# Performance work log

Hardware: AMD Instinct MI355X
Metric: run time of the kernel (lower is better)

Reference implementation:

```python
import jax, jax.numpy as jnp
import numpy as np

B, L = 1, 2048
D_MODEL, D_STATE, D_CONV, EXPAND = 512, 16, 4, 2
D_INNER = D_MODEL * EXPAND
EPS = 1e-10  # clamp used by the torch reference


def setup_inputs() -> dict:
    key = jax.random.key(0)
    ks = jax.random.split(key, 8)
    s = lambda fan: 1.0 / np.sqrt(fan)
    x = jax.random.normal(ks[0], (B, L, D_MODEL), jnp.float32)
    # Weights stored in (in, out) layout: y = x @ W  (equivalent to torch Linear with W.T)
    W_in = jax.random.normal(ks[1], (D_MODEL, 2 * D_INNER), jnp.float32) * s(D_MODEL)
    conv_w = jax.random.normal(ks[2], (D_INNER, 1, D_CONV), jnp.float32) * s(D_CONV)  # depthwise (O, I/groups, K)
    conv_b = jax.random.normal(ks[3], (D_INNER,), jnp.float32) * 0.01
    W_xproj = jax.random.normal(ks[4], (D_INNER, 2 * D_STATE + 1), jnp.float32) * s(D_INNER)
    dt_w = jax.random.normal(ks[5], (D_INNER,), jnp.float32) * 0.1  # Linear(1, d_inner) weight, squeezed
    dt_b = jax.random.normal(ks[6], (D_INNER,), jnp.float32) * 0.1 - 2.0  # keep delta smallish
    A_log = jnp.log(jnp.arange(1, D_STATE + 1, dtype=jnp.float32))
    D = jnp.ones((D_INNER,), jnp.float32)
    W_out = jax.random.normal(ks[7], (D_INNER, D_MODEL), jnp.float32) * s(D_INNER)
    return {"x": x, "W_in": W_in, "conv_w": conv_w, "conv_b": conv_b,
            "W_xproj": W_xproj, "dt_w": dt_w, "dt_b": dt_b,
            "A_log": A_log, "D": D, "W_out": W_out}


def reference(x, W_in, conv_w, conv_b, W_xproj, dt_w, dt_b, A_log, D, W_out):
    d_inner, _, d_conv = conv_w.shape
    d_state = A_log.shape[0]

    xz = x @ W_in                                    # (B, L, 2*d_inner)
    xs, z = jnp.split(xz, 2, axis=-1)

    # Depthwise causal conv1d: left-pad d_conv-1 == torch pad-both + truncate to L
    xc = jnp.transpose(xs, (0, 2, 1))                # (B, d_inner, L)
    xc = jax.lax.conv_general_dilated(
        xc, conv_w, window_strides=(1,), padding=[(d_conv - 1, 0)],
        feature_group_count=d_inner,
        dimension_numbers=("NCH", "OIH", "NCH")) + conv_b[None, :, None]
    xs = jax.nn.silu(jnp.transpose(xc, (0, 2, 1)))   # (B, L, d_inner)

    xp = xs @ W_xproj                                # (B, L, 2*d_state+1)
    delta = jax.nn.softplus(xp[..., 0:1] * dt_w + dt_b)  # (B, L, d_inner)
    Bp = xp[..., 1:1 + d_state]                      # (B, L, d_state)
    Cp = xp[..., 1 + d_state:]                       # (B, L, d_state)
    A = -jnp.exp(A_log)                              # (d_state,)

    # --- parallel selective scan via cumulative log-sum (faithful to source) ---
    A_bar = jnp.exp(delta[..., None] * A)                            # (B,L,Di,S)
    BX = delta[..., None] * Bp[:, :, None, :] * xs[..., None]        # (B,L,Di,S)
    log_A_bar = jnp.log(jnp.maximum(A_bar, EPS))
    A_cumsum = jnp.exp(jnp.cumsum(log_A_bar, axis=1))
    A_shift = jnp.concatenate([jnp.ones_like(A_cumsum[:, :1]), A_cumsum[:, :-1]], axis=1)
    weighted_BX = BX / jnp.maximum(A_shift, EPS)
    h = A_cumsum * jnp.cumsum(weighted_BX, axis=1) / jnp.maximum(A_bar, EPS)
    y = jnp.einsum("bls,blds->bld", Cp, h) + D * xs                  # (B,L,Di)

    y = y * jax.nn.silu(z)
    return y @ W_out                                                  # (B,L,D)
```

## Files before the change

kernel.cpp:

```cpp
#include <hip/hip_runtime.h>
#include <hip/hip_bf16.h>


#define L_SEQ 2048
#define DM 512
#define DI 1024
#define DS 16
#define NXP 33
#define EPS 1e-10f
#define RCPEPS 1e10f
#define LOG2E 1.44269504088896340736f
#define LN2 0.69314718055994530942f
#define LOG2EPS -33.219280948873623478f

typedef __hip_bfloat16 bf16;
typedef __attribute__((ext_vector_type(8))) short bf16x8v;
typedef __attribute__((ext_vector_type(4))) float f32x4v;
typedef __attribute__((ext_vector_type(4))) unsigned int u32x4v;

__device__ __forceinline__ float ldf(const float* p) { return *p; }
__device__ __forceinline__ float ldf(const bf16* p) { return __bfloat162float(*p); }

__device__ __forceinline__ void st1(float* p, float v) { *p = v; }
__device__ __forceinline__ void st1(bf16* p, float v) { *p = __float2bfloat16(v); }

__device__ __forceinline__ float fexp2(float x) { return __builtin_amdgcn_exp2f(x); }
__device__ __forceinline__ float frcp(float x) { return __builtin_amdgcn_rcpf(x); }

__device__ __forceinline__ void load8(const float* p, float* v) {
  float4 a = *(const float4*)p;
  float4 b = *(const float4*)(p + 4);
  v[0] = a.x; v[1] = a.y; v[2] = a.z; v[3] = a.w;
  v[4] = b.x; v[5] = b.y; v[6] = b.z; v[7] = b.w;
}
__device__ __forceinline__ void load8(const bf16* p, float* v) {
  bf16 t[8];
  *(uint4*)t = *(const uint4*)p;
#pragma unroll
  for (int j = 0; j < 8; ++j) v[j] = __bfloat162float(t[j]);
}

__global__ __launch_bounds__(256)
void transpose_cast_kernel(const float* __restrict__ W, bf16* __restrict__ WT,
                           int R, int C) {
  __shared__ float tile[32][33];
  int c0 = blockIdx.x * 32, r0 = blockIdx.y * 32;
  int tx = threadIdx.x & 31, ty = threadIdx.x >> 5;
#pragma unroll
  for (int i = 0; i < 4; ++i) {
    int rr = ty + i * 8;
    tile[rr][tx] = W[(size_t)(r0 + rr) * C + c0 + tx];
  }
  __syncthreads();
#pragma unroll
  for (int i = 0; i < 4; ++i) {
    int cc = ty + i * 8;
    WT[(size_t)(c0 + cc) * R + r0 + tx] = __float2bfloat16(tile[tx][cc]);
  }
}

__global__ __launch_bounds__(256)
void cast_f32_bf16_kernel(const float* __restrict__ src, bf16* __restrict__ dst,
                          int n8) {
  int i = blockIdx.x * 256 + threadIdx.x;
  if (i < n8) {
    float v[8];
    load8(src + (size_t)i * 8, v);
    bf16 o[8];
#pragma unroll
    for (int j = 0; j < 8; ++j) o[j] = __float2bfloat16(v[j]);
    *(uint4*)(dst + (size_t)i * 8) = *(uint4*)o;
  }
}

template <typename TA, typename TC>
__global__ __launch_bounds__(256)
void gemm_bt64(const TA* __restrict__ A, const bf16* __restrict__ BT,
               TC* __restrict__ C, int M, int N, int K, int lda, int ldc) {
  __shared__ __align__(16) bf16 As[64 * 40];
  __shared__ __align__(16) bf16 Bs[64 * 40];
  const int tid = threadIdx.x;
  const int wave = tid >> 6, lane = tid & 63;
  const int q = lane >> 4, r = lane & 15;
  const int row0 = blockIdx.y * 64, col0 = blockIdx.x * 64;
  const int srow = tid >> 2, sseg = tid & 3;
  f32x4v acc[4] = {};
  for (int k0 = 0; k0 < K; k0 += 32) {
    if constexpr (sizeof(TA) == 2) {
      *(uint4*)&As[srow * 40 + sseg * 8] =
          *(const uint4*)(A + (size_t)(row0 + srow) * lda + k0 + sseg * 8);
    } else {
      float v[8];
      load8(A + (size_t)(row0 + srow) * lda + k0 + sseg * 8, v);
      bf16* dst = &As[srow * 40 + sseg * 8];
#pragma unroll
      for (int j = 0; j < 8; ++j) dst[j] = __float2bfloat16(v[j]);
    }
    *(uint4*)&Bs[srow * 40 + sseg * 8] =
        *(const uint4*)(BT + (size_t)(col0 + srow) * K + k0 + sseg * 8);
    __syncthreads();
    bf16x8v a = *(const bf16x8v*)&As[(wave * 16 + r) * 40 + q * 8];
#pragma unroll
    for (int j = 0; j < 4; ++j) {
      bf16x8v b = *(const bf16x8v*)&Bs[(j * 16 + r) * 40 + q * 8];
      acc[j] = __builtin_amdgcn_mfma_f32_16x16x32_bf16(a, b, acc[j], 0, 0, 0);
    }
    __syncthreads();
  }
#pragma unroll
  for (int j = 0; j < 4; ++j)
#pragma unroll
    for (int reg = 0; reg < 4; ++reg) {
      int m = row0 + wave * 16 + q * 4 + reg;
      int n = col0 + j * 16 + r;
      st1(C + (size_t)m * ldc + n, acc[j][reg]);
    }
}

__global__ __launch_bounds__(256)
void gemm_xproj(const bf16* __restrict__ A, const float* __restrict__ Wx,
                float* __restrict__ xpcT) {
  __shared__ __align__(16) bf16 As[64 * 40];
  __shared__ __align__(16) bf16 Bs[64 * 40];
  const int tid = threadIdx.x;
  const int wave = tid >> 6, lane = tid & 63;
  const int q = lane >> 4, r = lane & 15;
  const int row0 = blockIdx.y * 64;
  const int srow = tid >> 2, sseg = tid & 3;
  f32x4v acc[4] = {};
  for (int k0 = 0; k0 < DI; k0 += 32) {
    *(uint4*)&As[srow * 40 + sseg * 8] =
        *(const uint4*)(A + (size_t)(row0 + srow) * DI + k0 + sseg * 8);
    int k = tid >> 3, n0 = (tid & 7) * 8;
#pragma unroll
    for (int j = 0; j < 8; ++j) {
      int n = n0 + j;
      float v = (n < NXP) ? Wx[(size_t)(k0 + k) * NXP + n] : 0.f;
      Bs[n * 40 + k] = __float2bfloat16(v);
    }
    __syncthreads();
    bf16x8v a = *(const bf16x8v*)&As[(wave * 16 + r) * 40 + q * 8];
#pragma unroll
    for (int j = 0; j < 4; ++j) {
      bf16x8v b = *(const bf16x8v*)&Bs[(j * 16 + r) * 40 + q * 8];
      acc[j] = __builtin_amdgcn_mfma_f32_16x16x32_bf16(a, b, acc[j], 0, 0, 0);
    }
    __syncthreads();
  }
#pragma unroll
  for (int j = 0; j < 4; ++j)
#pragma unroll
    for (int reg = 0; reg < 4; ++reg) {
      int m = row0 + wave * 16 + q * 4 + reg;
      int n = j * 16 + r;
      if (n < NXP) xpcT[(size_t)n * L_SEQ + m] = acc[j][reg];
    }
}

__global__ __launch_bounds__(256)
void conv_silu_dual(const bf16* __restrict__ xz, const float* __restrict__ conv_w,
                    const float* __restrict__ conv_b, bf16* __restrict__ xs,
                    bf16* __restrict__ xsT) {
  __shared__ bf16 tile[67][72];
  __shared__ bf16 sout[64][72];
  const int tid = threadIdx.x;
  const int d0 = blockIdx.x * 64, l0 = blockIdx.y * 64;
  for (int slot = tid; slot < 67 * 8; slot += 256) {
    int rr = slot >> 3, seg = slot & 7;
    int l = l0 - 3 + rr;
    uint4 v = {0, 0, 0, 0};
    if (l >= 0) v = *(const uint4*)(xz + (size_t)l * (2 * DI) + d0 + seg * 8);
    *(uint4*)&tile[rr][seg * 8] = v;
  }
  __syncthreads();
  {
    int lr = tid >> 3, c0t = (tid & 7) * 8;
#pragma unroll
    for (int half = 0; half < 2; ++half) {
      int lrow = lr + half * 32;
      bf16 o[8];
#pragma unroll
      for (int j = 0; j < 8; ++j) {
        int c = c0t + j;
        float acc = conv_b[d0 + c];
#pragma unroll
        for (int k = 0; k < 4; ++k)
          acc = fmaf(__bfloat162float(tile[lrow + k][c]), conv_w[(d0 + c) * 4 + k], acc);
        float v = acc / (1.f + __expf(-acc));
        o[j] = __float2bfloat16(v);
        sout[c][lrow] = o[j];
      }
      *(uint4*)(xs + (size_t)(l0 + lrow) * DI + d0 + c0t) = *(uint4*)o;
    }
  }
  __syncthreads();
  for (int slot = tid; slot < 64 * 8; slot += 256) {
    int dd = slot >> 3, seg = slot & 7;
    *(uint4*)(xsT + (size_t)(d0 + dd) * L_SEQ + l0 + seg * 8) =
        *(uint4*)&sout[dd][seg * 8];
  }
}

__global__ __launch_bounds__(256)
void gate_transpose_kernel(const bf16* __restrict__ yT, const bf16* __restrict__ zbuf,
                           int ldz, bf16* __restrict__ ys) {
  __shared__ bf16 tile[64][72];
  int d0 = blockIdx.y * 64, l0 = blockIdx.x * 64;
#pragma unroll
  for (int it = 0; it < 2; ++it) {
    int slot = threadIdx.x + it * 256;
    int dd = slot >> 3, seg = slot & 7;
    *(uint4*)&tile[dd][seg * 8] = *(const uint4*)(yT + (size_t)(d0 + dd) * L_SEQ + l0 + seg * 8);
  }
  __syncthreads();
#pragma unroll
  for (int it = 0; it < 2; ++it) {
    int slot = threadIdx.x + it * 256;
    int ll = slot >> 3, seg = slot & 7;
    bf16 zt[8];
    *(uint4*)zt = *(const uint4*)(zbuf + (size_t)(l0 + ll) * ldz + d0 + seg * 8);
    bf16 o[8];
#pragma unroll
    for (int j = 0; j < 8; ++j) {
      float yv = __bfloat162float(tile[seg * 8 + j][ll]);
      float zv = __bfloat162float(zt[j]);
      o[j] = __float2bfloat16(yv * zv * frcp(1.f + fexp2(-zv * LOG2E)));
    }
    *(uint4*)(ys + (size_t)(l0 + ll) * DI + d0 + seg * 8) = *(uint4*)o;
  }
}

#define LC 512
#define NW 16
#define SPW 32
#define PSX 513
#define LCP 516

__global__ __launch_bounds__(1024)
void scan_kernel(bf16* __restrict__ xsT, const float* __restrict__ xpcT,
                 const float* __restrict__ dt_w, const float* __restrict__ dt_b,
                 const float* __restrict__ A_log, const float* __restrict__ Dvec) {
  __shared__ float sxpT[NXP * PSX];
  __shared__ float sdt[4 * LCP], sg[4 * LCP], sxs[4 * LCP];
  __shared__ float sys[4 * LCP];
  __shared__ float Wtot[NW][64], Vtot[NW][64];
  const int tid = threadIdx.x;
  const int wave = tid >> 6, lane = tid & 63;
  const int s = lane & 15, dl = lane >> 4;
  const int d0 = blockIdx.x * 4;
  const int base = wave * SPW;
  const float As2 = -expf(A_log[s]) * LOG2E;
  const float Dd = Dvec[d0 + dl];
  float dtw[4], dtb[4];
#pragma unroll
  for (int c = 0; c < 4; ++c) {
    dtw[c] = dt_w[d0 + c];
    dtb[c] = dt_b[d0 + c];
  }
  float cs2_carry = 0.f, S_carry = 0.f;
  for (int l0 = 0; l0 < L_SEQ; l0 += LC) {
    for (int idx = tid; idx < NXP * LC; idx += 1024) {
      int u = __builtin_amdgcn_readfirstlane(idx & ~63);
      int j = u >> 9, lb = u & (LC - 1);
      const float* gp = xpcT + (size_t)j * L_SEQ + l0 + lb + lane;
      __builtin_amdgcn_global_load_lds(
          (const __attribute__((address_space(1))) void*)gp,
          (__attribute__((address_space(3))) void*)&sxpT[j * PSX + lb], 4, 0, 0);
    }
    for (int slot = tid; slot < 4 * (LC / 8); slot += 1024) {
      int c = slot >> 6, seg = slot & 63;
      bf16 tmp[8];
      *(uint4*)tmp = *(const uint4*)(xsT + (size_t)(d0 + c) * L_SEQ + l0 + seg * 8);
#pragma unroll
      for (int j = 0; j < 8; ++j) sxs[c * LCP + seg * 8 + j] = __bfloat162float(tmp[j]);
    }
    __syncthreads();
    for (int idx = tid; idx < 4 * LC; idx += 1024) {
      int c = idx >> 9, i = idx & (LC - 1);
      float x0 = sxpT[i];
      float a = fmaf(x0, dtw[c], dtb[c]);
      float dt = __log2f(1.f + fexp2(a * LOG2E)) * LN2;
      sdt[c * LCP + i] = dt;
      sg[c * LCP + i] = dt * sxs[c * LCP + i];
    }
    __syncthreads();
    float P[SPW];
    float Wl = 0.f;
#pragma unroll
    for (int k = 0; k < SPW; ++k) {
      float u = sdt[dl * LCP + base + k] * As2;
      P[k] = Wl;
      Wl += fmaxf(u, LOG2EPS);
    }
    Wtot[wave][lane] = Wl;
    __syncthreads();
    float O = cs2_carry, Wall = 0.f;
    for (int w = 0; w < NW; ++w) {
      float t = Wtot[w][lane];
      if (w < wave) O += t;
      Wall += t;
    }
    float Vl = 0.f;
#pragma unroll
    for (int k = 0; k < SPW; ++k) {
      float rcpA = fminf(fexp2(-(O + P[k])), RCPEPS);
      float gb = sg[dl * LCP + base + k] * sxpT[(1 + s) * PSX + base + k];
      Vl = fmaf(gb, rcpA, Vl);
    }
    Vtot[wave][lane] = Vl;
    __syncthreads();
    float SO = S_carry, Vall = 0.f;
    for (int w = 0; w < NW; ++w) {
      float tv = Vtot[w][lane];
      if (w < wave) SO += tv;
      Vall += tv;
    }
    float S = SO;
#pragma unroll
    for (int k = 0; k < SPW; ++k) {
      float xk = O + P[k];
      float rcpA = fminf(fexp2(-xk), RCPEPS);
      float aprev = fexp2(xk);
      float gb = sg[dl * LCP + base + k] * sxpT[(1 + s) * PSX + base + k];
      S = fmaf(gb, rcpA, S);
      float h = aprev * S;
      float contrib = sxpT[(17 + s) * PSX + base + k] * h;
      contrib += __shfl_xor(contrib, 8);
      contrib += __shfl_xor(contrib, 4);
      contrib += __shfl_xor(contrib, 2);
      contrib += __shfl_xor(contrib, 1);
      if (s == 0)
        sys[dl * LCP + base + k] = contrib + Dd * sxs[dl * LCP + base + k];
    }
    cs2_carry += Wall;
    S_carry += Vall;
    __syncthreads();
    for (int slot = tid; slot < 4 * (LC / 8); slot += 1024) {
      int c = slot >> 6, seg = slot & 63;
      bf16 tmp[8];
#pragma unroll
      for (int j = 0; j < 8; ++j) tmp[j] = __float2bfloat16(sys[c * LCP + seg * 8 + j]);
      u32x4v vv;
      vv.x = ((unsigned int*)tmp)[0]; vv.y = ((unsigned int*)tmp)[1];
      vv.z = ((unsigned int*)tmp)[2]; vv.w = ((unsigned int*)tmp)[3];
      __builtin_nontemporal_store(vv,
          (u32x4v*)(xsT + (size_t)(d0 + c) * L_SEQ + l0 + seg * 8));
    }
  }
}

extern "C" void kernel_launch(void* const* d_in, const int* in_sizes, int n_in,
                              void* d_out, int out_size, void* d_ws, size_t ws_size,
                              hipStream_t stream) {
  const float* x       = (const float*)d_in[0];
  const float* W_in    = (const float*)d_in[1];
  const float* conv_w  = (const float*)d_in[2];
  const float* conv_b  = (const float*)d_in[3];
  const float* W_xproj = (const float*)d_in[4];
  const float* dt_w    = (const float*)d_in[5];
  const float* dt_b    = (const float*)d_in[6];
  const float* A_log   = (const float*)d_in[7];
  const float* Dvec    = (const float*)d_in[8];
  const float* W_out   = (const float*)d_in[9];
  float* out = (float*)d_out;

  char* ws = (char*)d_ws;
  const size_t MB = 1024 * 1024;
  bf16* xz    = (bf16*)(ws);
  bf16* buf1  = (bf16*)(ws + 8 * MB);
  bf16* WinT  = (bf16*)(ws + 12 * MB);
  bf16* xbf   = (bf16*)(ws + 14 * MB);
  bf16* xsT   = (bf16*)(ws + 12 * MB);
  bf16* WoutT = (bf16*)(ws + 12 * MB);
  float* xpcT = (float*)(ws + 16 * MB);

  transpose_cast_kernel<<<dim3(2 * DI / 32, DM / 32), 256, 0, stream>>>(
      W_in, WinT, DM, 2 * DI);
  cast_f32_bf16_kernel<<<dim3(L_SEQ * DM / (256 * 8)), 256, 0, stream>>>(
      x, xbf, L_SEQ * DM / 8);
  gemm_bt64<bf16, bf16><<<dim3(2 * DI / 64, L_SEQ / 64), 256, 0, stream>>>(
      xbf, WinT, xz, L_SEQ, 2 * DI, DM, DM, 2 * DI);
  conv_silu_dual<<<dim3(DI / 64, L_SEQ / 64), 256, 0, stream>>>(
      xz, conv_w, conv_b, buf1, xsT);
  gemm_xproj<<<dim3(1, L_SEQ / 64), 256, 0, stream>>>(buf1, W_xproj, xpcT);
  scan_kernel<<<DI / 4, 1024, 0, stream>>>(xsT, xpcT, dt_w, dt_b, A_log, Dvec);
  gate_transpose_kernel<<<dim3(L_SEQ / 64, DI / 64), 256, 0, stream>>>(
      xsT, xz + DI, 2 * DI, buf1);
  transpose_cast_kernel<<<dim3(DM / 32, DI / 32), 256, 0, stream>>>(
      W_out, WoutT, DI, DM);
  gemm_bt64<bf16, float><<<dim3(DM / 64, L_SEQ / 64), 256, 0, stream>>>(
      buf1, WoutT, out, L_SEQ, DM, DI, DI, DM);
}
```

Baseline: 221.4 us.

## Replace GEMM with double-buffered direct-to-LDS loads and larger per-wave tiles

Replaces the simple 64x64 bf16 MFMA GEMM with a templated kernel that uses global_load_lds to copy tiles straight into double-buffered shared memory. This overlaps the next K-tile's load with the current MFMAs and removes one barrier per iteration. The in-projection now uses 128x128 block tiles with 4x4 MFMA tiles per wave for more reuse, while the out-projection keeps 64x64 tiles. The change removes LDS padding, which may introduce bank conflicts, and drops the fp32-input path.

```diff
diff --git a/kernel.cpp b/kernel.cpp
--- a/kernel.cpp
+++ b/kernel.cpp
@@ -18,9 +18,6 @@
 typedef __attribute__((ext_vector_type(4))) float f32x4v;
 typedef __attribute__((ext_vector_type(4))) unsigned int u32x4v;
 
-__device__ __forceinline__ float ldf(const float* p) { return *p; }
-__device__ __forceinline__ float ldf(const bf16* p) { return __bfloat162float(*p); }
-
 __device__ __forceinline__ void st1(float* p, float v) { *p = v; }
 __device__ __forceinline__ void st1(bf16* p, float v) { *p = __float2bfloat16(v); }
 
@@ -32,12 +29,6 @@
   float4 b = *(const float4*)(p + 4);
   v[0] = a.x; v[1] = a.y; v[2] = a.z; v[3] = a.w;
   v[4] = b.x; v[5] = b.y; v[6] = b.z; v[7] = b.w;
-}
-__device__ __forceinline__ void load8(const bf16* p, float* v) {
-  bf16 t[8];
-  *(uint4*)t = *(const uint4*)p;
-#pragma unroll
-  for (int j = 0; j < 8; ++j) v[j] = __bfloat162float(t[j]);
 }
 
 __global__ __launch_bounds__(256)
@@ -73,48 +64,76 @@
   }
 }
 
-template <typename TA, typename TC>
-__global__ __launch_bounds__(256)
-void gemm_bt64(const TA* __restrict__ A, const bf16* __restrict__ BT,
-               TC* __restrict__ C, int M, int N, int K, int lda, int ldc) {
-  __shared__ __align__(16) bf16 As[64 * 40];
-  __shared__ __align__(16) bf16 Bs[64 * 40];
+template <int WM, int WN, typename TC>
+__global__ __launch_bounds__(256)
+void gemm_gl(const bf16* __restrict__ A, const bf16* __restrict__ BT,
+             TC* __restrict__ C, int K, int lda, int ldc) {
+  constexpr int BM = 2 * WM * 16, BN = 2 * WN * 16;
+  __shared__ __align__(16) bf16 As[2][BM * 32];
+  __shared__ __align__(16) bf16 Bs[2][BN * 32];
   const int tid = threadIdx.x;
   const int wave = tid >> 6, lane = tid & 63;
   const int q = lane >> 4, r = lane & 15;
-  const int row0 = blockIdx.y * 64, col0 = blockIdx.x * 64;
-  const int srow = tid >> 2, sseg = tid & 3;
-  f32x4v acc[4] = {};
-  for (int k0 = 0; k0 < K; k0 += 32) {
-    if constexpr (sizeof(TA) == 2) {
-      *(uint4*)&As[srow * 40 + sseg * 8] =
-          *(const uint4*)(A + (size_t)(row0 + srow) * lda + k0 + sseg * 8);
-    } else {
-      float v[8];
-      load8(A + (size_t)(row0 + srow) * lda + k0 + sseg * 8, v);
-      bf16* dst = &As[srow * 40 + sseg * 8];
-#pragma unroll
-      for (int j = 0; j < 8; ++j) dst[j] = __float2bfloat16(v[j]);
-    }
-    *(uint4*)&Bs[srow * 40 + sseg * 8] =
-        *(const uint4*)(BT + (size_t)(col0 + srow) * K + k0 + sseg * 8);
-    __syncthreads();
-    bf16x8v a = *(const bf16x8v*)&As[(wave * 16 + r) * 40 + q * 8];
-#pragma unroll
-    for (int j = 0; j < 4; ++j) {
-      bf16x8v b = *(const bf16x8v*)&Bs[(j * 16 + r) * 40 + q * 8];
-      acc[j] = __builtin_amdgcn_mfma_f32_16x16x32_bf16(a, b, acc[j], 0, 0, 0);
-    }
-    __syncthreads();
-  }
-#pragma unroll
-  for (int j = 0; j < 4; ++j)
-#pragma unroll
-    for (int reg = 0; reg < 4; ++reg) {
-      int m = row0 + wave * 16 + q * 4 + reg;
-      int n = col0 + j * 16 + r;
-      st1(C + (size_t)m * ldc + n, acc[j][reg]);
-    }
+  const int wr = wave >> 1, wc = wave & 1;
+  const int row0 = blockIdx.y * BM, col0 = blockIdx.x * BN;
+  f32x4v acc[WM][WN] = {};
+  const int nt = K / 32;
+
+  auto stage = [&](int buf, int t) {
+    int k0 = t * 32;
+#pragma unroll
+    for (int i = 0; i < BM / 64; ++i) {
+      int slot = tid + i * 256;
+      int row = slot >> 2, seg = slot & 3;
+      __builtin_amdgcn_global_load_lds(
+          (const __attribute__((address_space(1))) void*)(
+              A + (size_t)(row0 + row) * lda + k0 + seg * 8),
+          (__attribute__((address_space(3))) void*)&As[buf][row * 32 + seg * 8],
+          16, 0, 0);
+    }
+#pragma unroll
+    for (int i = 0; i < BN / 64; ++i) {
+      int slot = tid + i * 256;
+      int row = slot >> 2, seg = slot & 3;
+      __builtin_amdgcn_global_load_lds(
+          (const __attribute__((address_space(1))) void*)(
+              BT + (size_t)(col0 + row) * K + k0 + seg * 8),
+          (__attribute__((address_space(3))) void*)&Bs[buf][row * 32 + seg * 8],
+          16, 0, 0);
+    }
+  };
+
+  stage(0, 0);
+  __syncthreads();
+  int cur = 0;
+  for (int t = 0; t < nt; ++t) {
+    if (t + 1 < nt) stage(cur ^ 1, t + 1);
+    bf16x8v a[WM], b[WN];
+#pragma unroll
+    for (int m = 0; m < WM; ++m)
+      a[m] = *(const bf16x8v*)&As[cur][(wr * WM * 16 + m * 16 + r) * 32 + q * 8];
+#pragma unroll
+    for (int n = 0; n < WN; ++n)
+      b[n] = *(const bf16x8v*)&Bs[cur][(wc * WN * 16 + n * 16 + r) * 32 + q * 8];
+#pragma unroll
+    for (int m = 0; m < WM; ++m)
+#pragma unroll
+      for (int n = 0; n < WN; ++n)
+        acc[m][n] = __builtin_amdgcn_mfma_f32_16x16x32_bf16(a[m], b[n],
+                                                            acc[m][n], 0, 0, 0);
+    __syncthreads();
+    cur ^= 1;
+  }
+#pragma unroll
+  for (int m = 0; m < WM; ++m)
+#pragma unroll
+    for (int n = 0; n < WN; ++n)
+#pragma unroll
+      for (int reg = 0; reg < 4; ++reg) {
+        int mm = row0 + wr * WM * 16 + m * 16 + q * 4 + reg;
+        int nn = col0 + wc * WN * 16 + n * 16 + r;
+        st1(C + (size_t)mm * ldc + nn, acc[m][n][reg]);
+      }
 }
 
 __global__ __launch_bounds__(256)
@@ -378,8 +397,8 @@
       W_in, WinT, DM, 2 * DI);
   cast_f32_bf16_kernel<<<dim3(L_SEQ * DM / (256 * 8)), 256, 0, stream>>>(
       x, xbf, L_SEQ * DM / 8);
-  gemm_bt64<bf16, bf16><<<dim3(2 * DI / 64, L_SEQ / 64), 256, 0, stream>>>(
-      xbf, WinT, xz, L_SEQ, 2 * DI, DM, DM, 2 * DI);
+  gemm_gl<4, 4, bf16><<<dim3(2 * DI / 128, L_SEQ / 128), 256, 0, stream>>>(
+      xbf, WinT, xz, DM, DM, 2 * DI);
   conv_silu_dual<<<dim3(DI / 64, L_SEQ / 64), 256, 0, stream>>>(
       xz, conv_w, conv_b, buf1, xsT);
   gemm_xproj<<<dim3(1, L_SEQ / 64), 256, 0, stream>>>(buf1, W_xproj, xpcT);
@@ -388,6 +407,6 @@
       xsT, xz + DI, 2 * DI, buf1);
   transpose_cast_kernel<<<dim3(DM / 32, DI / 32), 256, 0, stream>>>(
       W_out, WoutT, DI, DM);
-  gemm_bt64<bf16, float><<<dim3(DM / 64, L_SEQ / 64), 256, 0, stream>>>(
-      buf1, WoutT, out, L_SEQ, DM, DI, DI, DM);
-}
+  gemm_gl<2, 2, float><<<dim3(DM / 64, L_SEQ / 64), 256, 0, stream>>>(
+      buf1, WoutT, out, DI, DI, DM);
+}
```

Result: no change. 218.6 us (-1.3%).
